# Kernel optimization log

Hardware: AMD Instinct MI355X
Metric: run time of the kernel (lower is better)

The kernel has to match this reference:

```python
import jax, jax.numpy as jnp
import numpy as np

HIDDEN = 2048
NH = 32          # num attention heads
NKV = 8          # num key/value heads
HD = HIDDEN // NH  # head_dim = 64
ROPE_BASE = 10000.0
NEG_INF = -1e9


def _rope_interleaved(t, positions):
    # t: [b, s, h, d], interleaved RoPE over full head_dim (flash-attn RotaryEmbedding(interleaved=True))
    d = t.shape[-1]
    inv_freq = 1.0 / (ROPE_BASE ** (jnp.arange(0, d, 2, dtype=jnp.float32) / d))
    ang = positions[:, None].astype(jnp.float32) * inv_freq[None, :]  # [s, d/2]
    cos = jnp.cos(ang)[None, :, None, :]
    sin = jnp.sin(ang)[None, :, None, :]
    t1 = t[..., 0::2]
    t2 = t[..., 1::2]
    out_even = t1 * cos - t2 * sin
    out_odd = t1 * sin + t2 * cos
    return jnp.stack([out_even, out_odd], axis=-1).reshape(t.shape)


def setup_inputs() -> dict:
    key = jax.random.key(0)
    k1, k2, k3 = jax.random.split(key, 3)
    B, S = 2, 2048
    x = jax.random.normal(k1, (B, S, HIDDEN), dtype=jnp.float32)
    mask = jnp.ones((B, S), dtype=jnp.int32)  # padding mask, all valid
    total_head_dim = (NH + 2 * NKV) * HD  # 3072
    scale = 1.0 / np.sqrt(HIDDEN)
    w_qkv = jax.random.normal(k2, (HIDDEN, total_head_dim), dtype=jnp.float32) * scale
    w_o = jax.random.normal(k3, (NH * HD, HIDDEN), dtype=jnp.float32) * scale
    return {"x": x, "mask": mask, "w_qkv": w_qkv, "w_o": w_o}


def reference(x, mask, w_qkv, w_o):
    B, S, _ = x.shape
    kv_size = NKV * HD
    qkv = jnp.einsum('bsh,hd->bsd', x, w_qkv)
    q = qkv[..., :HIDDEN].reshape(B, S, NH, HD)
    kv = qkv[..., HIDDEN:].reshape(B, S, 2, NKV, HD)
    pos = jnp.arange(S)  # seqlen_offset = 0 (input_pos None)
    q = _rope_interleaved(q, pos)
    k = _rope_interleaved(kv[:, :, 0], pos)
    v = kv[:, :, 1]
    # GQA: expand kv heads to NH
    groups = NH // NKV
    k = jnp.repeat(k, groups, axis=2)  # [b, s, NH, HD]
    v = jnp.repeat(v, groups, axis=2)
    scores = jnp.einsum('bqhd,bkhd->bhqk', q, k) / np.sqrt(HD)
    causal = jnp.tril(jnp.ones((S, S), dtype=bool))
    key_valid = mask[:, None, None, :] > 0  # [b,1,1,k]
    scores = jnp.where(causal[None, None] & key_valid, scores, NEG_INF)
    probs = jax.nn.softmax(scores, axis=-1)
    attn = jnp.einsum('bhqk,bkhd->bqhd', probs, v)
    # pad_input writes zeros at padded query positions
    attn = attn * (mask[:, :, None, None] > 0)
    attn = attn.reshape(B, S, NH * HD)
    return jnp.einsum('bsd,dh->bsh', attn, w_o)
```

## Files before the change

kernel.cpp:

```cpp
#include <hip/hip_runtime.h>
#include <hip/hip_bf16.h>
#include <cstdint>
#include <cstddef>

typedef __attribute__((ext_vector_type(8))) short bf16x8;
typedef __attribute__((ext_vector_type(4))) float f32x4;

static constexpr int CB  = 2;
static constexpr int CS  = 2048;
static constexpr int CH  = 2048;
static constexpr int CNH = 32;
static constexpr int CNKV = 8;
static constexpr int CHD = 64;
static constexpr int CTHD = 3072;

__device__ __forceinline__ void gload_lds16(const void* g, void* l) {
  __builtin_amdgcn_global_load_lds(
      (const __attribute__((address_space(1))) unsigned int*)g,
      (__attribute__((address_space(3))) unsigned int*)l, 16, 0, 0);
}

__device__ __forceinline__ unsigned short bfbits(float f) {
  __hip_bfloat16 h = __float2bfloat16(f);
  return *(unsigned short*)&h;
}

__global__ void conv_bf16(const float* __restrict__ in, __hip_bfloat16* __restrict__ out, int n) {
  const int i = (blockIdx.x * 256 + threadIdx.x) * 4;
  if (i >= n) return;
  const float4 v = *(const float4*)(in + i);
  out[i]     = __float2bfloat16(v.x);
  out[i + 1] = __float2bfloat16(v.y);
  out[i + 2] = __float2bfloat16(v.z);
  out[i + 3] = __float2bfloat16(v.w);
}

__global__ __launch_bounds__(256) void transpose_conv(const float* __restrict__ in,
                                                      __hip_bfloat16* __restrict__ out,
                                                      int R, int Cc) {
  __shared__ float t[32][33];
  const int nbx = Cc >> 5;
  const int bx = blockIdx.x % nbx, by = blockIdx.x / nbx;
  const int c0 = bx << 5, r0 = by << 5;
  const int tx = threadIdx.x & 31, ty = threadIdx.x >> 5;
#pragma unroll
  for (int j = 0; j < 32; j += 8)
    t[ty + j][tx] = in[(size_t)(r0 + ty + j) * Cc + c0 + tx];
  __syncthreads();
#pragma unroll
  for (int j = 0; j < 32; j += 8)
    out[(size_t)(c0 + ty + j) * R + r0 + tx] = __float2bfloat16(t[tx][ty + j]);
}

template <typename OutT>
__global__ __launch_bounds__(512) void gemm_ph(const __hip_bfloat16* __restrict__ A,
                                               const __hip_bfloat16* __restrict__ Bt,
                                               OutT* __restrict__ C, int M, int N, int K) {
  __shared__ __hip_bfloat16 As[2][128 * 64];
  __shared__ __hip_bfloat16 Bs[2][256 * 64];
  const int tid = threadIdx.x;
  const int lane = tid & 63;
  const int wave = tid >> 6;
  const int nTn = N >> 8;
  const int nwg = gridDim.x;
  const int wg = (blockIdx.x & 7) * (nwg >> 3) + (blockIdx.x >> 3);
  const int tm = wg / nTn, tn = wg % nTn;
  const size_t m0 = (size_t)tm * 128, n0 = (size_t)tn * 256;
  const __hip_bfloat16* Ag = A + m0 * K;
  const __hip_bfloat16* Bg = Bt + n0 * K;
  const int wr = wave >> 2, wc = wave & 3;
  const int rsel = lane & 15, hi = lane >> 4;

  f32x4 acc[4][4];
#pragma unroll
  for (int mf = 0; mf < 4; ++mf)
#pragma unroll
    for (int nf = 0; nf < 4; ++nf) acc[mf][nf] = (f32x4){0.f, 0.f, 0.f, 0.f};

  auto stageA = [&](int u) {
    const int k0 = u << 6, buf = u & 1;
#pragma unroll
    for (int i = 0; i < 2; ++i) {
      const int c = i * 512 + tid;
      const int r = c >> 3;
      const int swz = ((c & 7) ^ (r & 7)) << 3;
      gload_lds16(Ag + (size_t)r * K + k0 + swz, &As[buf][(i * 512 + wave * 64) * 8]);
    }
  };
  auto stageB = [&](int u) {
    const int k0 = u << 6, buf = u & 1;
#pragma unroll
    for (int i = 0; i < 4; ++i) {
      const int c = i * 512 + tid;
      const int r = c >> 3;
      const int swz = ((c & 7) ^ (r & 7)) << 3;
      gload_lds16(Bg + (size_t)r * K + k0 + swz, &Bs[buf][(i * 512 + wave * 64) * 8]);
    }
  };

  bf16x8 af[4][2];
  auto readA = [&](int buf) {
#pragma unroll
    for (int mf = 0; mf < 4; ++mf) {
      const int row = wr * 64 + mf * 16 + rsel;
      const int r7 = row & 7;
      af[mf][0] = *(const bf16x8*)&As[buf][row * 64 + ((hi ^ r7) << 3)];
      af[mf][1] = *(const bf16x8*)&As[buf][row * 64 + (((4 | hi) ^ r7) << 3)];
    }
  };
  auto mm = [&](int buf, int nfb) {
    bf16x8 bfr[2][2];
#pragma unroll
    for (int nf = 0; nf < 2; ++nf) {
      const int row = wc * 64 + (nfb + nf) * 16 + rsel;
      const int r7 = row & 7;
      bfr[nf][0] = *(const bf16x8*)&Bs[buf][row * 64 + ((hi ^ r7) << 3)];
      bfr[nf][1] = *(const bf16x8*)&Bs[buf][row * 64 + (((4 | hi) ^ r7) << 3)];
    }
    __builtin_amdgcn_s_setprio(1);
#pragma unroll
    for (int mf = 0; mf < 4; ++mf)
#pragma unroll
      for (int nf = 0; nf < 2; ++nf)
#pragma unroll
        for (int kk = 0; kk < 2; ++kk)
          acc[mf][nfb + nf] =
              __builtin_amdgcn_mfma_f32_16x16x32_bf16(af[mf][kk], bfr[nf][kk], acc[mf][nfb + nf], 0, 0, 0);
    __builtin_amdgcn_s_setprio(0);
  };

  const int T = K >> 7;
  const int UMAX = 2 * T;
  stageA(0); stageB(0); stageA(1); stageB(1);

  for (int t = 0; t < T; ++t) {
    const int u0 = 2 * t, u1 = 2 * t + 1;
    asm volatile("s_waitcnt vmcnt(2)" ::: "memory");
    __builtin_amdgcn_sched_barrier(0);
    __builtin_amdgcn_s_barrier();
    __builtin_amdgcn_sched_barrier(0);
    if (t >= 1) stageB(u1);
    readA(0);
    mm(0, 0);
    __builtin_amdgcn_sched_barrier(0);
    __builtin_amdgcn_s_barrier();
    __builtin_amdgcn_sched_barrier(0);
    if (u0 + 2 < UMAX) stageA(u0 + 2);
    mm(0, 2);
    if (t == T - 1) {
      asm volatile("s_waitcnt vmcnt(0)" ::: "memory");
    } else {
      asm volatile("s_waitcnt vmcnt(2)" ::: "memory");
    }
    __builtin_amdgcn_sched_barrier(0);
    __builtin_amdgcn_s_barrier();
    __builtin_amdgcn_sched_barrier(0);
    if (u0 + 2 < UMAX) stageB(u0 + 2);
    readA(1);
    mm(1, 0);
    __builtin_amdgcn_sched_barrier(0);
    __builtin_amdgcn_s_barrier();
    __builtin_amdgcn_sched_barrier(0);
    if (u1 + 2 < UMAX) stageA(u1 + 2);
    mm(1, 2);
  }

  const int rowb = hi << 2;
#pragma unroll
  for (int mf = 0; mf < 4; ++mf)
#pragma unroll
    for (int nf = 0; nf < 4; ++nf) {
      const size_t r0 = m0 + wr * 64 + mf * 16 + rowb;
      const size_t cc = n0 + wc * 64 + nf * 16 + rsel;
#pragma unroll
      for (int j = 0; j < 4; ++j) {
        const float v = acc[mf][nf][j];
        if constexpr (sizeof(OutT) == 4)
          C[(r0 + j) * N + cc] = v;
        else
          C[(r0 + j) * N + cc] = __float2bfloat16(v);
      }
    }
}

__global__ void rope_extract(const __hip_bfloat16* __restrict__ qkv,
                             __hip_bfloat16* __restrict__ Q,
                             __hip_bfloat16* __restrict__ Kr) {
  const int idx = blockIdx.x * 256 + threadIdx.x;
  const int i = idx & 31;
  const int hs = (idx >> 5) % 40;
  const int r = idx / (40 * 32);
  const int srow = r & (CS - 1);
  const int b = r >> 11;
  const float inv = exp2f(-(float)i * (13.287712379549449f / 32.0f));
  const float ang = (float)srow * inv;
  const float sn = sinf(ang), cs = cosf(ang);
  const int col = (hs < CNH) ? hs * CHD + 2 * i : CH + (hs - CNH) * CHD + 2 * i;
  const float t1 = __bfloat162float(qkv[(size_t)r * CTHD + col]);
  const float t2 = __bfloat162float(qkv[(size_t)r * CTHD + col + 1]);
  const float scl = (hs < CNH) ? 0.18033688011112042f : 1.0f;
  const float ev = (t1 * cs - t2 * sn) * scl;
  const float ov = (t1 * sn + t2 * cs) * scl;
  __hip_bfloat16* dst;
  if (hs < CNH)
    dst = Q + ((((size_t)b * CNH + hs) * CS + srow) * CHD + 2 * i);
  else
    dst = Kr + ((((size_t)b * CNKV + (hs - CNH)) * CS + srow) * CHD + 2 * i);
  dst[0] = __float2bfloat16(ev);
  dst[1] = __float2bfloat16(ov);
}

__global__ __launch_bounds__(256) void v_transpose(const __hip_bfloat16* __restrict__ qkv,
                                                   __hip_bfloat16* __restrict__ VT) {
  __shared__ __hip_bfloat16 t[64][72];
  const int bi = blockIdx.x;
  const int stile = bi & 31;
  const int kvh = (bi >> 5) & 7;
  const int b = bi >> 8;
  const int tx = threadIdx.x & 63;
  const int ty = threadIdx.x >> 6;
  const int s0 = stile * 64;
#pragma unroll
  for (int j = 0; j < 16; ++j) {
    const int sl = ty * 16 + j;
    t[sl][tx] = qkv[(size_t)(b * CS + s0 + sl) * CTHD + (CH + CNKV * CHD) + kvh * CHD + tx];
  }
  __syncthreads();
#pragma unroll
  for (int j = 0; j < 16; ++j) {
    const int dl = ty * 16 + j;
    VT[(((size_t)b * CNKV + kvh) * CHD + dl) * CS + s0 + tx] = t[tx][dl];
  }
}

__global__ __launch_bounds__(256) void attn_fa(const __hip_bfloat16* __restrict__ Q,
                                               const __hip_bfloat16* __restrict__ Kr,
                                               const __hip_bfloat16* __restrict__ VT,
                                               const int* __restrict__ mask,
                                               __hip_bfloat16* __restrict__ O) {
  __shared__ __hip_bfloat16 Ks[2][64 * 64];
  __shared__ __hip_bfloat16 Vs[64 * 64];
  __shared__ __hip_bfloat16 P4[4][16][72];
  const int kvh = blockIdx.x & 7;
  const int slot = blockIdx.x >> 3;
  const int qw = 127 - (slot >> 1);
  const int b = slot & 1;
  const int tid = threadIdx.x;
  const int wave = tid >> 6, lane = tid & 63;
  const int h = kvh * 4 + wave;
  const int q0 = qw * 16;
  const int rsel = lane & 15;
  const int hi = lane >> 4;
  const int k8 = hi * 8;
  const int rowb = hi * 4;
  const int qr = q0 + rsel;
  const __hip_bfloat16* Qp = Q + (((size_t)b * CNH + h) * CS + q0) * CHD;
  const __hip_bfloat16* Kp = Kr + ((size_t)b * CNKV + kvh) * CS * CHD;
  const __hip_bfloat16* Vp = VT + ((size_t)b * CNKV + kvh) * CHD * CS;
  const int* mp = mask + b * CS;
  __hip_bfloat16(*P)[72] = P4[wave];

  bf16x8 qf[2];
  qf[0] = *(const bf16x8*)(Qp + rsel * CHD + k8);
  qf[1] = *(const bf16x8*)(Qp + rsel * CHD + 32 + k8);

  f32x4 o[4];
#pragma unroll
  for (int nt = 0; nt < 4; ++nt) o[nt] = (f32x4){0.f, 0.f, 0.f, 0.f};
  float mrun = -3e38f, lrun = 0.f;

  const int nkb = (qw >> 2) + 1;

  auto stageK = [&](int buf, int key0) {
#pragma unroll
    for (int half = 0; half < 2; ++half) {
      const int c = half * 256 + tid;
      const int r = c >> 3;
      const int swz = ((c & 7) ^ (r & 7)) * 8;
      gload_lds16(Kp + (size_t)(key0 + r) * CHD + swz,
                  &Ks[buf][(half * 256 + wave * 64) * 8]);
    }
  };
  auto stageV = [&](int key0) {
#pragma unroll
    for (int half = 0; half < 2; ++half) {
      const int c = half * 256 + tid;
      const int r = c >> 3;
      const int swz = ((c & 7) ^ (r & 7)) * 8;
      gload_lds16(Vp + (size_t)r * CS + key0 + swz,
                  &Vs[(half * 256 + wave * 64) * 8]);
    }
  };

  int mcur = mp[lane], mnext = 0;
  stageK(0, 0);
  __syncthreads();

  for (int t = 0; t < nkb; ++t) {
    const int cur = t & 1;
    const int key0 = t * 64;
    const bool last = (t == nkb - 1);
    stageV(key0);
    if (!last) {
      stageK(cur ^ 1, key0 + 64);
      mnext = mp[key0 + 64 + lane];
    }
    const unsigned long long kvbits = __ballot(mcur > 0);
    const int sz = rsel & 7;
    bf16x8 kc[8];
#pragma unroll
    for (int kt = 0; kt < 4; ++kt) {
      const int row = (kt * 16 + rsel) * 64;
      kc[kt * 2]     = *(const bf16x8*)&Ks[cur][row + ((hi ^ sz) << 3)];
      kc[kt * 2 + 1] = *(const bf16x8*)&Ks[cur][row + (((hi ^ 4) ^ sz) << 3)];
    }
    f32x4 st[4];
#pragma unroll
    for (int kt = 0; kt < 4; ++kt) {
      f32x4 s = (f32x4){0.f, 0.f, 0.f, 0.f};
      s = __builtin_amdgcn_mfma_f32_16x16x32_bf16(kc[kt * 2], qf[0], s, 0, 0, 0);
      s = __builtin_amdgcn_mfma_f32_16x16x32_bf16(kc[kt * 2 + 1], qf[1], s, 0, 0, 0);
      st[kt] = s;
    }
    if (!(kvbits == ~0ull && !last)) {
#pragma unroll
      for (int kt = 0; kt < 4; ++kt)
#pragma unroll
        for (int j = 0; j < 4; ++j) {
          const int idx = kt * 16 + rowb + j;
          const bool bad = !((kvbits >> idx) & 1ull) || (last && key0 + idx > qr);
          if (bad) st[kt][j] = -1e9f;
        }
    }
    float pmax = st[0][0];
#pragma unroll
    for (int kt = 0; kt < 4; ++kt)
#pragma unroll
      for (int j = 0; j < 4; ++j) pmax = fmaxf(pmax, st[kt][j]);
    pmax = fmaxf(pmax, __shfl_xor(pmax, 16));
    pmax = fmaxf(pmax, __shfl_xor(pmax, 32));
    if (__any(pmax > mrun + 8.0f)) {
      const float mn = fmaxf(mrun, pmax);
      const float al = exp2f(mrun - mn);
      mrun = mn;
      lrun *= al;
#pragma unroll
      for (int nt = 0; nt < 4; ++nt)
#pragma unroll
        for (int j = 0; j < 4; ++j) o[nt][j] *= al;
    }
    float ps = 0.f;
#pragma unroll
    for (int kt = 0; kt < 4; ++kt)
#pragma unroll
      for (int j = 0; j < 4; ++j) {
        const float p = exp2f(st[kt][j] - mrun);
        st[kt][j] = p;
        ps += p;
      }
    ps += __shfl_xor(ps, 16);
    ps += __shfl_xor(ps, 32);
    lrun += ps;
#pragma unroll
    for (int kt = 0; kt < 4; ++kt) {
      ushort4 pk;
      pk.x = bfbits(st[kt][0]);
      pk.y = bfbits(st[kt][1]);
      pk.z = bfbits(st[kt][2]);
      pk.w = bfbits(st[kt][3]);
      *(ushort4*)&P[rsel][kt * 16 + rowb] = pk;
    }
    __syncthreads();
    const bf16x8 pb0 = *(const bf16x8*)&P[rsel][k8];
    const bf16x8 pb1 = *(const bf16x8*)&P[rsel][32 + k8];
    bf16x8 vf[8];
#pragma unroll
    for (int nt = 0; nt < 4; ++nt) {
      const int row = (nt * 16 + rsel) * 64;
      vf[nt * 2]     = *(const bf16x8*)&Vs[row + ((hi ^ sz) << 3)];
      vf[nt * 2 + 1] = *(const bf16x8*)&Vs[row + (((hi ^ 4) ^ sz) << 3)];
    }
#pragma unroll
    for (int nt = 0; nt < 4; ++nt) {
      o[nt] = __builtin_amdgcn_mfma_f32_16x16x32_bf16(vf[nt * 2], pb0, o[nt], 0, 0, 0);
      o[nt] = __builtin_amdgcn_mfma_f32_16x16x32_bf16(vf[nt * 2 + 1], pb1, o[nt], 0, 0, 0);
    }
    __syncthreads();
    mcur = mnext;
  }

  const float qm = (mp[qr] > 0) ? 1.0f : 0.0f;
  const float inv = qm / fmaxf(lrun, 1e-20f);
  __hip_bfloat16* Orow = O + (((size_t)b * CS + qr) * CNH + h) * CHD;
#pragma unroll
  for (int nt = 0; nt < 4; ++nt) {
    ushort4 ok;
    ok.x = bfbits(o[nt][0] * inv);
    ok.y = bfbits(o[nt][1] * inv);
    ok.z = bfbits(o[nt][2] * inv);
    ok.w = bfbits(o[nt][3] * inv);
    *(ushort4*)(Orow + nt * 16 + rowb) = ok;
  }
}

extern "C" void kernel_launch(void* const* d_in, const int* in_sizes, int n_in,
                              void* d_out, int out_size, void* d_ws, size_t ws_size,
                              hipStream_t stream) {
  const float* x = (const float*)d_in[0];
  const int* mask = (const int*)d_in[1];
  const float* w_qkv = (const float*)d_in[2];
  const float* w_o = (const float*)d_in[3];
  float* out = (float*)d_out;

  char* ws = (char*)d_ws;
  size_t off = 0;
  auto alloc = [&](size_t bytes) {
    char* p = ws + off;
    off += (bytes + 255) & ~(size_t)255;
    return p;
  };
  const size_t M = (size_t)CB * CS;
  __hip_bfloat16* x_bf  = (__hip_bfloat16*)alloc(M * CH * 2);
  __hip_bfloat16* wqkvT = (__hip_bfloat16*)alloc((size_t)CTHD * CH * 2);
  __hip_bfloat16* woT   = (__hip_bfloat16*)alloc((size_t)CH * CH * 2);
  __hip_bfloat16* qkv   = (__hip_bfloat16*)alloc(M * CTHD * 2);
  __hip_bfloat16* Qb    = (__hip_bfloat16*)alloc((size_t)CB * CNH * CS * CHD * 2);
  __hip_bfloat16* Kb    = (__hip_bfloat16*)alloc((size_t)CB * CNKV * CS * CHD * 2);
  __hip_bfloat16* VTb   = (__hip_bfloat16*)alloc((size_t)CB * CNKV * CHD * CS * 2);
  __hip_bfloat16* attnb = (__hip_bfloat16*)alloc(M * CH * 2);

  conv_bf16<<<(int)(M * CH / 4 / 256), 256, 0, stream>>>(x, x_bf, (int)(M * CH));
  transpose_conv<<<(CTHD / 32) * (CH / 32), 256, 0, stream>>>(w_qkv, wqkvT, CH, CTHD);
  transpose_conv<<<(CH / 32) * (CH / 32), 256, 0, stream>>>(w_o, woT, CH, CH);
  gemm_ph<__hip_bfloat16><<<(int)(M / 128) * (CTHD / 256), 512, 0, stream>>>(
      x_bf, wqkvT, qkv, (int)M, CTHD, CH);
  rope_extract<<<(int)(M * 40 * 32 / 256), 256, 0, stream>>>(qkv, Qb, Kb);
  v_transpose<<<CB * CNKV * 32, 256, 0, stream>>>(qkv, VTb);
  attn_fa<<<CB * CNKV * 128, 256, 0, stream>>>(Qb, Kb, VTb, mask, attnb);
  gemm_ph<float><<<(int)(M / 128) * (CH / 256), 512, 0, stream>>>(
      attnb, woT, out, (int)M, CH, CH);
}
```

Measured before the change: 235.2 us.

## Process two 16-row query subtiles per wave with 2-wave attention blocks

Each wave now handles 32 query rows (two 16-row subtiles) for one head, and each block has two waves covering two of the four GQA heads. K and V fragments loaded from LDS are reused across both subtiles, halving LDS fragment reads per query. Per-K-tile staging and barrier costs are amortized over more MFMA work. The trade-off is more registers per wave, fewer waves per block, and a causal tile granularity of 32 rows, which adds some masked work on diagonal tiles.

```diff
diff --git a/kernel.cpp b/kernel.cpp
--- a/kernel.cpp
+++ b/kernel.cpp
@@ -233,62 +233,64 @@
   }
 }
 
-__global__ __launch_bounds__(256) void attn_fa(const __hip_bfloat16* __restrict__ Q,
+__global__ __launch_bounds__(128) void attn_fa(const __hip_bfloat16* __restrict__ Q,
                                                const __hip_bfloat16* __restrict__ Kr,
                                                const __hip_bfloat16* __restrict__ VT,
                                                const int* __restrict__ mask,
                                                __hip_bfloat16* __restrict__ O) {
   __shared__ __hip_bfloat16 Ks[2][64 * 64];
   __shared__ __hip_bfloat16 Vs[64 * 64];
-  __shared__ __hip_bfloat16 P4[4][16][72];
+  __shared__ __hip_bfloat16 P4[2][2][16][72];
   const int kvh = blockIdx.x & 7;
   const int slot = blockIdx.x >> 3;
-  const int qw = 127 - (slot >> 1);
-  const int b = slot & 1;
+  const int qw = 63 - (slot >> 2);
+  const int b = (slot >> 1) & 1;
+  const int hp = slot & 1;
   const int tid = threadIdx.x;
   const int wave = tid >> 6, lane = tid & 63;
-  const int h = kvh * 4 + wave;
-  const int q0 = qw * 16;
+  const int h = kvh * 4 + hp * 2 + wave;
+  const int q0 = qw * 32;
   const int rsel = lane & 15;
   const int hi = lane >> 4;
   const int k8 = hi * 8;
   const int rowb = hi * 4;
-  const int qr = q0 + rsel;
   const __hip_bfloat16* Qp = Q + (((size_t)b * CNH + h) * CS + q0) * CHD;
   const __hip_bfloat16* Kp = Kr + ((size_t)b * CNKV + kvh) * CS * CHD;
   const __hip_bfloat16* Vp = VT + ((size_t)b * CNKV + kvh) * CHD * CS;
   const int* mp = mask + b * CS;
-  __hip_bfloat16(*P)[72] = P4[wave];
-
-  bf16x8 qf[2];
-  qf[0] = *(const bf16x8*)(Qp + rsel * CHD + k8);
-  qf[1] = *(const bf16x8*)(Qp + rsel * CHD + 32 + k8);
-
-  f32x4 o[4];
-#pragma unroll
-  for (int nt = 0; nt < 4; ++nt) o[nt] = (f32x4){0.f, 0.f, 0.f, 0.f};
-  float mrun = -3e38f, lrun = 0.f;
-
-  const int nkb = (qw >> 2) + 1;
+
+  bf16x8 qf[2][2];
+#pragma unroll
+  for (int s = 0; s < 2; ++s) {
+    qf[s][0] = *(const bf16x8*)(Qp + (s * 16 + rsel) * CHD + k8);
+    qf[s][1] = *(const bf16x8*)(Qp + (s * 16 + rsel) * CHD + 32 + k8);
+  }
+
+  f32x4 o[2][4];
+#pragma unroll
+  for (int s = 0; s < 2; ++s)
+#pragma unroll
+    for (int nt = 0; nt < 4; ++nt) o[s][nt] = (f32x4){0.f, 0.f, 0.f, 0.f};
+  float mrun[2] = {-3e38f, -3e38f}, lrun[2] = {0.f, 0.f};
+
+  const int nkb = (qw >> 1) + 1;
 
   auto stageK = [&](int buf, int key0) {
 #pragma unroll
-    for (int half = 0; half < 2; ++half) {
-      const int c = half * 256 + tid;
+    for (int i = 0; i < 4; ++i) {
+      const int c = i * 128 + tid;
       const int r = c >> 3;
       const int swz = ((c & 7) ^ (r & 7)) * 8;
-      gload_lds16(Kp + (size_t)(key0 + r) * CHD + swz,
-                  &Ks[buf][(half * 256 + wave * 64) * 8]);
+      gload_lds16(Kp + (size_t)(key0 + r) * CHD + swz, &Ks[buf][c * 8]);
     }
   };
   auto stageV = [&](int key0) {
 #pragma unroll
-    for (int half = 0; half < 2; ++half) {
-      const int c = half * 256 + tid;
+    for (int i = 0; i < 4; ++i) {
+      const int c = i * 128 + tid;
       const int r = c >> 3;
       const int swz = ((c & 7) ^ (r & 7)) * 8;
-      gload_lds16(Vp + (size_t)r * CS + key0 + swz,
-                  &Vs[(half * 256 + wave * 64) * 8]);
+      gload_lds16(Vp + (size_t)r * CS + key0 + swz, &Vs[c * 8]);
     }
   };
 
@@ -314,65 +316,76 @@
       kc[kt * 2]     = *(const bf16x8*)&Ks[cur][row + ((hi ^ sz) << 3)];
       kc[kt * 2 + 1] = *(const bf16x8*)&Ks[cur][row + (((hi ^ 4) ^ sz) << 3)];
     }
-    f32x4 st[4];
+    f32x4 st[2][4];
 #pragma unroll
     for (int kt = 0; kt < 4; ++kt) {
-      f32x4 s = (f32x4){0.f, 0.f, 0.f, 0.f};
-      s = __builtin_amdgcn_mfma_f32_16x16x32_bf16(kc[kt * 2], qf[0], s, 0, 0, 0);
-      s = __builtin_amdgcn_mfma_f32_16x16x32_bf16(kc[kt * 2 + 1], qf[1], s, 0, 0, 0);
-      st[kt] = s;
-    }
-    if (!(kvbits == ~0ull && !last)) {
+#pragma unroll
+      for (int s = 0; s < 2; ++s) {
+        f32x4 a = (f32x4){0.f, 0.f, 0.f, 0.f};
+        a = __builtin_amdgcn_mfma_f32_16x16x32_bf16(kc[kt * 2], qf[s][0], a, 0, 0, 0);
+        a = __builtin_amdgcn_mfma_f32_16x16x32_bf16(kc[kt * 2 + 1], qf[s][1], a, 0, 0, 0);
+        st[s][kt] = a;
+      }
+    }
+#pragma unroll
+    for (int s = 0; s < 2; ++s) {
+      const int qs = q0 + s * 16;
+      const int qr = qs + rsel;
+      if (kvbits != ~0ull || key0 + 63 > qs) {
+#pragma unroll
+        for (int kt = 0; kt < 4; ++kt)
+#pragma unroll
+          for (int j = 0; j < 4; ++j) {
+            const int idx = kt * 16 + rowb + j;
+            const bool bad = !((kvbits >> idx) & 1ull) || (key0 + idx > qr);
+            if (bad) st[s][kt][j] = -1e9f;
+          }
+      }
+    }
+#pragma unroll
+    for (int s = 0; s < 2; ++s) {
+      float pmax = st[s][0][0];
 #pragma unroll
       for (int kt = 0; kt < 4; ++kt)
 #pragma unroll
+        for (int j = 0; j < 4; ++j) pmax = fmaxf(pmax, st[s][kt][j]);
+      pmax = fmaxf(pmax, __shfl_xor(pmax, 16));
+      pmax = fmaxf(pmax, __shfl_xor(pmax, 32));
+      if (__any(pmax > mrun[s] + 8.0f)) {
+        const float mn = fmaxf(mrun[s], pmax);
+        const float al = exp2f(mrun[s] - mn);
+        mrun[s] = mn;
+        lrun[s] *= al;
+#pragma unroll
+        for (int nt = 0; nt < 4; ++nt)
+#pragma unroll
+          for (int j = 0; j < 4; ++j) o[s][nt][j] *= al;
+      }
+      float ps = 0.f;
+#pragma unroll
+      for (int kt = 0; kt < 4; ++kt)
+#pragma unroll
         for (int j = 0; j < 4; ++j) {
-          const int idx = kt * 16 + rowb + j;
-          const bool bad = !((kvbits >> idx) & 1ull) || (last && key0 + idx > qr);
-          if (bad) st[kt][j] = -1e9f;
+          const float p = exp2f(st[s][kt][j] - mrun[s]);
+          st[s][kt][j] = p;
+          ps += p;
         }
-    }
-    float pmax = st[0][0];
-#pragma unroll
-    for (int kt = 0; kt < 4; ++kt)
-#pragma unroll
-      for (int j = 0; j < 4; ++j) pmax = fmaxf(pmax, st[kt][j]);
-    pmax = fmaxf(pmax, __shfl_xor(pmax, 16));
-    pmax = fmaxf(pmax, __shfl_xor(pmax, 32));
-    if (__any(pmax > mrun + 8.0f)) {
-      const float mn = fmaxf(mrun, pmax);
-      const float al = exp2f(mrun - mn);
-      mrun = mn;
-      lrun *= al;
-#pragma unroll
-      for (int nt = 0; nt < 4; ++nt)
-#pragma unroll
-        for (int j = 0; j < 4; ++j) o[nt][j] *= al;
-    }
-    float ps = 0.f;
-#pragma unroll
-    for (int kt = 0; kt < 4; ++kt)
-#pragma unroll
-      for (int j = 0; j < 4; ++j) {
-        const float p = exp2f(st[kt][j] - mrun);
-        st[kt][j] = p;
-        ps += p;
-      }
-    ps += __shfl_xor(ps, 16);
-    ps += __shfl_xor(ps, 32);
-    lrun += ps;
-#pragma unroll
-    for (int kt = 0; kt < 4; ++kt) {
-      ushort4 pk;
-      pk.x = bfbits(st[kt][0]);
-      pk.y = bfbits(st[kt][1]);
-      pk.z = bfbits(st[kt][2]);
-      pk.w = bfbits(st[kt][3]);
-      *(ushort4*)&P[rsel][kt * 16 + rowb] = pk;
-    }
+      ps += __shfl_xor(ps, 16);
+      ps += __shfl_xor(ps, 32);
+      lrun[s] += ps;
+    }
+#pragma unroll
+    for (int s = 0; s < 2; ++s)
+#pragma unroll
+      for (int kt = 0; kt < 4; ++kt) {
+        ushort4 pk;
+        pk.x = bfbits(st[s][kt][0]);
+        pk.y = bfbits(st[s][kt][1]);
+        pk.z = bfbits(st[s][kt][2]);
+        pk.w = bfbits(st[s][kt][3]);
+        *(ushort4*)&P4[wave][s][rsel][kt * 16 + rowb] = pk;
+      }
     __syncthreads();
-    const bf16x8 pb0 = *(const bf16x8*)&P[rsel][k8];
-    const bf16x8 pb1 = *(const bf16x8*)&P[rsel][32 + k8];
     bf16x8 vf[8];
 #pragma unroll
     for (int nt = 0; nt < 4; ++nt) {
@@ -380,26 +393,38 @@
       vf[nt * 2]     = *(const bf16x8*)&Vs[row + ((hi ^ sz) << 3)];
       vf[nt * 2 + 1] = *(const bf16x8*)&Vs[row + (((hi ^ 4) ^ sz) << 3)];
     }
-#pragma unroll
-    for (int nt = 0; nt < 4; ++nt) {
-      o[nt] = __builtin_amdgcn_mfma_f32_16x16x32_bf16(vf[nt * 2], pb0, o[nt], 0, 0, 0);
-      o[nt] = __builtin_amdgcn_mfma_f32_16x16x32_bf16(vf[nt * 2 + 1], pb1, o[nt], 0, 0, 0);
-    }
+    bf16x8 pb[2][2];
+#pragma unroll
+    for (int s = 0; s < 2; ++s) {
+      pb[s][0] = *(const bf16x8*)&P4[wave][s][rsel][k8];
+      pb[s][1] = *(const bf16x8*)&P4[wave][s][rsel][32 + k8];
+    }
+#pragma unroll
+    for (int nt = 0; nt < 4; ++nt)
+#pragma unroll
+      for (int s = 0; s < 2; ++s) {
+        o[s][nt] = __builtin_amdgcn_mfma_f32_16x16x32_bf16(vf[nt * 2], pb[s][0], o[s][nt], 0, 0, 0);
+        o[s][nt] = __builtin_amdgcn_mfma_f32_16x16x32_bf16(vf[nt * 2 + 1], pb[s][1], o[s][nt], 0, 0, 0);
+      }
     __syncthreads();
     mcur = mnext;
   }
 
-  const float qm = (mp[qr] > 0) ? 1.0f : 0.0f;
-  const float inv = qm / fmaxf(lrun, 1e-20f);
-  __hip_bfloat16* Orow = O + (((size_t)b * CS + qr) * CNH + h) * CHD;
-#pragma unroll
-  for (int nt = 0; nt < 4; ++nt) {
-    ushort4 ok;
-    ok.x = bfbits(o[nt][0] * inv);
-    ok.y = bfbits(o[nt][1] * inv);
-    ok.z = bfbits(o[nt][2] * inv);
-    ok.w = bfbits(o[nt][3] * inv);
-    *(ushort4*)(Orow + nt * 16 + rowb) = ok;
+#pragma unroll
+  for (int s = 0; s < 2; ++s) {
+    const int qr = q0 + s * 16 + rsel;
+    const float qm = (mp[qr] > 0) ? 1.0f : 0.0f;
+    const float inv = qm / fmaxf(lrun[s], 1e-20f);
+    __hip_bfloat16* Orow = O + (((size_t)b * CS + qr) * CNH + h) * CHD;
+#pragma unroll
+    for (int nt = 0; nt < 4; ++nt) {
+      ushort4 ok;
+      ok.x = bfbits(o[s][nt][0] * inv);
+      ok.y = bfbits(o[s][nt][1] * inv);
+      ok.z = bfbits(o[s][nt][2] * inv);
+      ok.w = bfbits(o[s][nt][3] * inv);
+      *(ushort4*)(Orow + nt * 16 + rowb) = ok;
+    }
   }
 }
 
@@ -436,7 +461,7 @@
       x_bf, wqkvT, qkv, (int)M, CTHD, CH);
   rope_extract<<<(int)(M * 40 * 32 / 256), 256, 0, stream>>>(qkv, Qb, Kb);
   v_transpose<<<CB * CNKV * 32, 256, 0, stream>>>(qkv, VTb);
-  attn_fa<<<CB * CNKV * 128, 256, 0, stream>>>(Qb, Kb, VTb, mask, attnb);
+  attn_fa<<<CB * CNKV * 128, 128, 0, stream>>>(Qb, Kb, VTb, mask, attnb);
   gemm_ph<float><<<(int)(M / 128) * (CH / 256), 512, 0, stream>>>(
       attnb, woT, out, (int)M, CH, CH);
 }
```

Result: slower. 286.4 us (+21.7%).
